# Kernel tuning notes

Measured on AMD Instinct MI355X. Metric: run time of the kernel, lower is better.

## Reference

```python
import jax, jax.numpy as jnp
import numpy as np
from jax import lax

B, T, N, H, NC = 2, 8, 512, 64, 10
NEG = -1e9
LN_EPS = 1e-5


def _gatv2(x, mask, Wl, Wr, att, b):
    # GATv2Conv (PyG semantics, eval mode): e_ij = att . leaky_relu(Wr x_i + Wl x_j),
    # softmax over source nodes j with self-loops, out_i = sum_j alpha_ij * (Wl x_j).
    # x: (B, N, Fin); mask: (N, N) bool adjacency incl. self-loops; att: (heads, C).
    heads, C = att.shape
    Bn, Nn, _ = x.shape
    xl = (x @ Wl).reshape(Bn, Nn, heads, C)  # source transform
    xr = (x @ Wr).reshape(Bn, Nn, heads, C)  # target transform
    s = jax.nn.leaky_relu(xr[:, :, None] + xl[:, None, :], 0.2)  # (B, Ni, Nj, h, C)
    e = jnp.einsum('bijhc,hc->bijh', s, att)
    e = jnp.where(mask[None, :, :, None], e, NEG)
    alpha = jax.nn.softmax(e, axis=2)  # softmax over neighbors j
    out = jnp.einsum('bijh,bjhc->bihc', alpha, xl)
    return out.reshape(Bn, Nn, heads * C) + b


def _gru_layer(x, Wih, Whh, bih, bhh):
    # torch nn.GRU single layer, batch_first; x: (B, T, Hin)
    h0 = jnp.zeros((x.shape[0], Whh.shape[0]), x.dtype)
    def step(h, xt):
        gi = xt @ Wih + bih
        gh = h @ Whh + bhh
        ir, iz, inn = jnp.split(gi, 3, axis=-1)
        hr, hz, hn = jnp.split(gh, 3, axis=-1)
        r = jax.nn.sigmoid(ir + hr)
        z = jax.nn.sigmoid(iz + hz)
        n = jnp.tanh(inn + r * hn)
        hnew = (1.0 - z) * n + z * h
        return hnew, hnew
    _, ys = lax.scan(step, h0, jnp.swapaxes(x, 0, 1))
    return jnp.swapaxes(ys, 0, 1)


def setup_inputs() -> dict:
    key = jax.random.key(0)
    ks = jax.random.split(key, 20)
    def rn(i, shape, s=0.1):
        return jax.random.normal(ks[i], shape, jnp.float32) * s
    x_seq = jax.random.normal(ks[0], (B, T, N, 1), jnp.float32)
    a = jax.random.uniform(ks[1], (N, N))
    up = jnp.triu((a > 0.95).astype(jnp.float32), 1)
    static_adj = up + up.T  # sparse symmetric 0/1 static graph
    dyn_W = jax.random.normal(ks[2], (N, N), jnp.float32)
    reg_lambda = jnp.array([0.05], jnp.float32)
    return {
        'x_seq': x_seq, 'static_adj': static_adj, 'dyn_W': dyn_W, 'reg_lambda': reg_lambda,
        'g1_Wl': rn(3, (1, H)), 'g1_Wr': rn(4, (1, H)), 'g1_att': rn(5, (4, H // 4)), 'g1_b': jnp.zeros(H),
        'g2_Wl': rn(6, (H, H)), 'g2_Wr': rn(7, (H, H)), 'g2_att': rn(8, (1, H)), 'g2_b': jnp.zeros(H),
        'gru_Wih0': rn(9, (H, 3 * H)), 'gru_Whh0': rn(10, (H, 3 * H)), 'gru_bih0': jnp.zeros(3 * H), 'gru_bhh0': jnp.zeros(3 * H),
        'gru_Wih1': rn(11, (H, 3 * H)), 'gru_Whh1': rn(12, (H, 3 * H)), 'gru_bih1': jnp.zeros(3 * H), 'gru_bhh1': jnp.zeros(3 * H),
        'attn_W': rn(13, (H, 1)), 'attn_b': jnp.zeros(1),
        'cls_W1': rn(14, (H, H)), 'cls_b1': jnp.zeros(H), 'ln_g': jnp.ones(H), 'ln_b': jnp.zeros(H),
        'cls_W2': rn(15, (H, NC)), 'cls_b2': jnp.zeros(NC),
    }


def reference(x_seq, static_adj, dyn_W, reg_lambda,
              g1_Wl, g1_Wr, g1_att, g1_b, g2_Wl, g2_Wr, g2_att, g2_b,
              gru_Wih0, gru_Whh0, gru_bih0, gru_bhh0,
              gru_Wih1, gru_Whh1, gru_bih1, gru_bhh1,
              attn_W, attn_b, cls_W1, cls_b1, ln_g, ln_b, cls_W2, cls_b2):
    Bn, Tn, Nn, _ = x_seq.shape
    lam = jnp.maximum(reg_lambda[0], 0.01)
    t = jnp.arange(Tn, dtype=x_seq.dtype)
    gts = jnp.exp(-lam * t)  # gating values per timestep
    dyn = jax.nn.relu(dyn_W + dyn_W.T)
    fused = gts[:, None, None] * static_adj + (1.0 - gts)[:, None, None] * dyn  # (T, N, N)
    masks = (fused > 0) | jnp.eye(Nn, dtype=bool)[None]  # edge set + self-loops

    def step(carry, inp):
        xt, mask = inp  # xt: (B, N, 1)
        h = jax.nn.elu(_gatv2(xt, mask, g1_Wl, g1_Wr, g1_att, g1_b))
        h = jax.nn.elu(_gatv2(h, mask, g2_Wl, g2_Wr, g2_att, g2_b))
        return carry, h.mean(axis=1)  # (B, H) graph readout

    _, reps = lax.scan(step, 0.0, (jnp.swapaxes(x_seq, 0, 1), masks))
    h_seq = jnp.swapaxes(reps, 0, 1)  # (B, T, H)

    gru_out = _gru_layer(h_seq, gru_Wih0, gru_Whh0, gru_bih0, gru_bhh0)
    gru_out = _gru_layer(gru_out, gru_Wih1, gru_Whh1, gru_bih1, gru_bhh1)

    att_scores = jax.nn.softmax((gru_out @ attn_W + attn_b)[..., 0], axis=1)  # (B, T)
    final = jnp.einsum('bt,bth->bh', att_scores, gru_out)

    z = final @ cls_W1 + cls_b1
    mu = jnp.mean(z, axis=-1, keepdims=True)
    var = jnp.var(z, axis=-1, keepdims=True)
    z = (z - mu) / jnp.sqrt(var + LN_EPS) * ln_g + ln_b
    z = jax.nn.gelu(z, approximate=False)
    logits = z @ cls_W2 + cls_b2
    return logits, gts, att_scores
```

## Files before the change

kernel.cpp:

```cpp
#include <hip/hip_runtime.h>
#include <math.h>

#define BB 2
#define TT 8
#define NN 512
#define HH 64
#define NC 10

typedef unsigned char uchar;

__device__ __forceinline__ float elu1(float v){ return v > 0.f ? v : expm1f(v); }
__device__ __forceinline__ float sigm(float v){ return 1.f/(1.f+expf(-v)); }

__global__ __launch_bounds__(256) void k_mask(
    const float* __restrict__ dW, const float* __restrict__ sadj,
    uchar* __restrict__ M0, uchar* __restrict__ M1,
    float* __restrict__ Z2, float* __restrict__ hseq,
    const float* __restrict__ att1, const float* __restrict__ Wr1,
    const float* __restrict__ Wl1, float* __restrict__ AB,
    const float* __restrict__ Whh0, const float* __restrict__ Wih1,
    const float* __restrict__ Whh1, float4* __restrict__ WT4)
{
    __shared__ float tr[64][65];
    int bx = blockIdx.x, by = blockIdx.y;
    int tid = threadIdx.x;
    if (blockIdx.z == 1){
        int idx = (by*8 + bx)*256 + tid;
        if (idx < 3*4096){
            int m = idx >> 12, r = idx & 4095;
            int gg = r >> 6, k = r & 63;
            const float* W = (m == 0) ? Whh0 : (m == 1) ? Wih1 : Whh1;
            float4 o;
            o.x = W[k*192 + gg];
            o.y = W[k*192 + 64 + gg];
            o.z = W[k*192 + 128 + gg];
            o.w = 0.f;
            WT4[(size_t)m*4096 + r] = o;
        }
        return;
    }
    int i0 = by*64, j0 = bx*64;
    #pragma unroll
    for (int q = 0; q < 4; ++q){
        int r = (tid >> 4) + 16*q, c4 = tid & 15;
        float4 v = *(const float4*)&dW[(size_t)(j0+r)*NN + i0 + 4*c4];
        tr[r][4*c4+0] = v.x; tr[r][4*c4+1] = v.y;
        tr[r][4*c4+2] = v.z; tr[r][4*c4+3] = v.w;
    }
    __syncthreads();
    #pragma unroll
    for (int q = 0; q < 4; ++q){
        int row = (tid >> 4) + 16*q, c4 = tid & 15;
        int i = i0 + row, j = j0 + 4*c4;
        float4 d  = *(const float4*)&dW[(size_t)i*NN + j];
        float4 sa = *(const float4*)&sadj[(size_t)i*NN + j];
        uchar4 m0, m1;
        float dd0 = d.x + tr[4*c4+0][row];
        float dd1 = d.y + tr[4*c4+1][row];
        float dd2 = d.z + tr[4*c4+2][row];
        float dd3 = d.w + tr[4*c4+3][row];
        m0.x = (sa.x > 0.f) || (i == j+0);
        m0.y = (sa.y > 0.f) || (i == j+1);
        m0.z = (sa.z > 0.f) || (i == j+2);
        m0.w = (sa.w > 0.f) || (i == j+3);
        m1.x = m0.x || (dd0 > 0.f);
        m1.y = m0.y || (dd1 > 0.f);
        m1.z = m0.z || (dd2 > 0.f);
        m1.w = m0.w || (dd3 > 0.f);
        *(uchar4*)&M0[(size_t)i*NN + j] = m0;
        *(uchar4*)&M1[(size_t)i*NN + j] = m1;
    }
    int flat = (by*8 + bx)*256 + tid;
    if (flat < BB*TT*NN) Z2[flat] = 0.f;
    else if (flat < BB*TT*NN + BB*TT*HH) hseq[flat - BB*TT*NN] = 0.f;
    if (bx == 0 && by == 0 && tid < 8){
        int h = tid & 3;
        const float* W = (tid < 4) ? Wr1 : Wl1;
        float s = 0.f;
        for (int c = 0; c < 16; ++c) s += att1[h*16+c]*W[h*16+c];
        AB[tid] = s;
    }
}

__global__ __launch_bounds__(256) void k_gat1f(
    const float* __restrict__ x_seq, const uchar* __restrict__ M0,
    const uchar* __restrict__ M1,
    const float* __restrict__ Wl, const float* __restrict__ Wr,
    const float* __restrict__ att, const float* __restrict__ bias,
    const float* __restrict__ AB,
    const float* __restrict__ Wl2, const float* __restrict__ Wr2,
    const float* __restrict__ att2,
    float* __restrict__ xl2, float* __restrict__ xr2,
    float* __restrict__ ui, float* __restrict__ vj)
{
    __shared__ float x_s[NN];
    __shared__ float S_s[4][4];
    __shared__ float h_s[4][HH];
    __shared__ float Wl2_s[64*64];
    __shared__ float Wr2_s[64*64];
    int bt = blockIdx.y; int t = bt % TT;
    int i0 = blockIdx.x * 4;
    int tid = threadIdx.x;
    int il = tid >> 6, jl = tid & 63;
    int i = i0 + il;
    const uchar* M = t ? M1 : M0;
    ((float2*)x_s)[tid] = ((const float2*)(x_seq + bt*NN))[tid];
    #pragma unroll
    for (int q = 0; q < 4; ++q){
        int idx = q*256 + tid;
        ((float4*)Wl2_s)[idx] = ((const float4*)Wl2)[idx];
        ((float4*)Wr2_s)[idx] = ((const float4*)Wr2)[idx];
    }
    __syncthreads();
    float xi = x_s[i];
    const uchar* Mrow = M + (size_t)i*NN;
    float xj[8], msk[8];
    #pragma unroll
    for (int jj = 0; jj < 8; ++jj){
        int j = jj*64 + jl;
        xj[jj] = x_s[j];
        msk[jj] = Mrow[j] ? 1.f : 0.f;
    }
    float sw[4] = {0,0,0,0}, swx[4] = {0,0,0,0};
    for (int h = 0; h < 4; ++h){
        float acc[8] = {0,0,0,0,0,0,0,0};
        #pragma unroll
        for (int c = 0; c < 16; ++c){
            int hc = h*16 + c;
            float wl = Wl[hc];
            float q  = 0.4f * att[hc];
            float pr = xi * Wr[hc];
            #pragma unroll
            for (int jj = 0; jj < 8; ++jj){
                float s = fmaf(xj[jj], wl, pr);
                acc[jj] = fmaf(q, fabsf(s), acc[jj]);
            }
        }
        float lin = 0.6f * xi * AB[h];
        float al6 = 0.6f * AB[4+h];
        #pragma unroll
        for (int jj = 0; jj < 8; ++jj){
            float e = acc[jj] + fmaf(al6, xj[jj], lin);
            float w = msk[jj] * __expf(e);
            sw[h] += w;
            swx[h] = fmaf(w, xj[jj], swx[h]);
        }
    }
    #pragma unroll
    for (int off = 32; off; off >>= 1){
        #pragma unroll
        for (int h = 0; h < 4; ++h){
            sw[h]  += __shfl_down(sw[h],  off);
            swx[h] += __shfl_down(swx[h], off);
        }
    }
    if (jl == 0){
        #pragma unroll
        for (int h = 0; h < 4; ++h) S_s[il][h] = swx[h] / sw[h];
    }
    __syncthreads();
    {
        int hc = tid & 63, row = tid >> 6;
        float v = S_s[row][hc >> 4] * Wl[hc] + bias[hc];
        h_s[row][hc] = elu1(v);
    }
    __syncthreads();
    {
        int c = tid & 63, row = tid >> 6;
        float al = 0.f, ar = 0.f;
        #pragma unroll 8
        for (int k = 0; k < 64; ++k){
            float hv = h_s[row][k];
            al = fmaf(hv, Wl2_s[k*64 + c], al);
            ar = fmaf(hv, Wr2_s[k*64 + c], ar);
        }
        size_t ridx = (size_t)(bt*NN + i0 + row);
        xl2[ridx*HH + c] = al;
        xr2[ridx*HH + c] = ar;
        float a2 = att2[c];
        float pu = a2 * ar, pv = a2 * al;
        #pragma unroll
        for (int off = 32; off; off >>= 1){
            pu += __shfl_down(pu, off);
            pv += __shfl_down(pv, off);
        }
        if (c == 0){ ui[ridx] = pu; vj[ridx] = pv; }
    }
}

__global__ __launch_bounds__(256) void k_e2(
    const float* __restrict__ xl2, const float* __restrict__ xr2,
    const uchar* __restrict__ M0, const uchar* __restrict__ M1,
    const float* __restrict__ att,
    const float* __restrict__ ui, const float* __restrict__ vj,
    float* __restrict__ WgT, float* __restrict__ Z2)
{
    __shared__ float xrT[64][68];
    __shared__ float xlT[64][68];
    int bt = blockIdx.z, t = bt % TT;
    int i0 = blockIdx.y*64, j0 = blockIdx.x*64;
    int base = bt*NN;
    int tid = threadIdx.x;
    const uchar* M = t ? M1 : M0;
    {
        int r = tid >> 2;
        #pragma unroll
        for (int q = 0; q < 4; ++q){
            int c4 = (tid & 3) + 4*q;
            float4 a = *(const float4*)&xr2[(size_t)(base+i0+r)*HH + 4*c4];
            float4 b = *(const float4*)&xl2[(size_t)(base+j0+r)*HH + 4*c4];
            xrT[4*c4+0][r] = a.x; xrT[4*c4+1][r] = a.y;
            xrT[4*c4+2][r] = a.z; xrT[4*c4+3][r] = a.w;
            xlT[4*c4+0][r] = b.x; xlT[4*c4+1][r] = b.y;
            xlT[4*c4+2][r] = b.z; xlT[4*c4+3][r] = b.w;
        }
    }
    int ti = tid >> 4, tj = tid & 15;
    int iL = ti*4, jL = tj*4;
    float4 u4 = *(const float4*)&ui[base+i0+iL];
    float4 v4 = *(const float4*)&vj[base+j0+jL];
    float uu[4] = {u4.x, u4.y, u4.z, u4.w};
    float vv[4] = {v4.x, v4.y, v4.z, v4.w};
    float acc[4][4];
    #pragma unroll
    for (int ii = 0; ii < 4; ++ii)
        #pragma unroll
        for (int jj = 0; jj < 4; ++jj)
            acc[ii][jj] = 0.6f*(uu[ii] + vv[jj]);
    __syncthreads();
    #pragma unroll 8
    for (int c = 0; c < 64; ++c){
        float qa = 0.4f * att[c];
        float4 a4 = *(const float4*)&xrT[c][iL];
        float4 b4 = *(const float4*)&xlT[c][jL];
        float a[4] = {a4.x, a4.y, a4.z, a4.w};
        float b[4] = {b4.x, b4.y, b4.z, b4.w};
        #pragma unroll
        for (int ii = 0; ii < 4; ++ii)
            #pragma unroll
            for (int jj = 0; jj < 4; ++jj)
                acc[ii][jj] = fmaf(qa, fabsf(a[ii] + b[jj]), acc[ii][jj]);
    }
    float w[4][4];
    #pragma unroll
    for (int ii = 0; ii < 4; ++ii){
        int i = i0 + iL + ii;
        uchar4 mr = *(const uchar4*)&M[(size_t)i*NN + j0 + jL];
        w[ii][0] = mr.x ? __expf(acc[ii][0]) : 0.f;
        w[ii][1] = mr.y ? __expf(acc[ii][1]) : 0.f;
        w[ii][2] = mr.z ? __expf(acc[ii][2]) : 0.f;
        w[ii][3] = mr.w ? __expf(acc[ii][3]) : 0.f;
    }
    #pragma unroll
    for (int jj = 0; jj < 4; ++jj){
        int j = j0 + jL + jj;
        float4 wv = { w[0][jj], w[1][jj], w[2][jj], w[3][jj] };
        *(float4*)&WgT[(size_t)(base+j)*NN + i0 + iL] = wv;
    }
    #pragma unroll
    for (int ii = 0; ii < 4; ++ii){
        float zi = w[ii][0] + w[ii][1] + w[ii][2] + w[ii][3];
        zi += __shfl_down(zi, 8);
        zi += __shfl_down(zi, 4);
        zi += __shfl_down(zi, 2);
        zi += __shfl_down(zi, 1);
        if (tj == 0) atomicAdd(&Z2[base + i0 + iL + ii], zi);
    }
}

__global__ __launch_bounds__(256) void k_a2(
    const float* __restrict__ WgT, const float* __restrict__ xl2,
    const float* __restrict__ Z2, const float* __restrict__ bias,
    float* __restrict__ hseq)
{
    __shared__ float a_s[64][20];
    __shared__ float x_s[64][68];
    __shared__ float msum[64];
    int bt = blockIdx.y;
    int i0 = blockIdx.x * 16;
    int base = bt * NN;
    int tid = threadIdx.x;
    int tg = tid >> 4, tc = tid & 15;
    if (tid < 64) msum[tid] = 0.f;
    float4 acc = {0,0,0,0};
    for (int jc = 0; jc < 8; ++jc){
        int j0 = jc*64;
        {
            int row = tid >> 2, c4 = tid & 3;
            ((float4*)&a_s[row][0])[c4] = ((const float4*)&WgT[(size_t)(base+j0+row)*NN + i0])[c4];
        }
        #pragma unroll
        for (int q = 0; q < 4; ++q){
            int idx = q*256 + tid; int row = idx >> 4, c4 = idx & 15;
            ((float4*)&x_s[row][0])[c4] = ((const float4*)&xl2[(size_t)(base+j0+row)*HH])[c4];
        }
        __syncthreads();
        #pragma unroll 8
        for (int j = 0; j < 64; ++j){
            float a = a_s[j][tg];
            float4 xv = ((float4*)&x_s[j][0])[tc];
            acc.x = fmaf(a, xv.x, acc.x);
            acc.y = fmaf(a, xv.y, acc.y);
            acc.z = fmaf(a, xv.z, acc.z);
            acc.w = fmaf(a, xv.w, acc.w);
        }
        __syncthreads();
    }
    float rz = 1.f / Z2[base + i0 + tg];
    float4 b4 = ((const float4*)bias)[tc];
    float4 h;
    h.x = elu1(acc.x*rz + b4.x);
    h.y = elu1(acc.y*rz + b4.y);
    h.z = elu1(acc.z*rz + b4.z);
    h.w = elu1(acc.w*rz + b4.w);
    atomicAdd(&msum[tc*4+0], h.x);
    atomicAdd(&msum[tc*4+1], h.y);
    atomicAdd(&msum[tc*4+2], h.z);
    atomicAdd(&msum[tc*4+3], h.w);
    __syncthreads();
    if (tid < 64) atomicAdd(&hseq[bt*HH + tid], msum[tid]*(1.f/(float)NN));
}

__global__ __launch_bounds__(256) void k_pre(
    const float* __restrict__ hseq, const float* __restrict__ Wih0,
    const float* __restrict__ bih0, float* __restrict__ gi0)
{
    int idx = blockIdx.x*256 + threadIdx.x;
    int bt = idx / 192, g = idx % 192;
    const float* x = hseq + bt*HH;
    float acc = bih0[g];
    #pragma unroll 8
    for (int k = 0; k < HH; ++k)
        acc = fmaf(x[k], Wih0[k*192 + g], acc);
    gi0[idx] = acc;
}

#define P4 65
__global__ __launch_bounds__(512) void k_gru2(
    const float* __restrict__ gi0, const float4* __restrict__ WT4,
    const float* __restrict__ bhh0,
    const float* __restrict__ bih1, const float* __restrict__ bhh1,
    const float* __restrict__ lamp, const float* __restrict__ attn_W,
    const float* __restrict__ attn_b, const float* __restrict__ W1,
    const float* __restrict__ b1, const float* __restrict__ ln_g,
    const float* __restrict__ ln_b, const float* __restrict__ W2,
    const float* __restrict__ b2, float* __restrict__ out)
{
    __shared__ float4 WA[64*P4];
    __shared__ float4 WB[64*P4];
    __shared__ float gi_s[BB*TT*192];
    __shared__ float y_s[BB*TT*HH];
    __shared__ float sc_s[BB][TT], at_s[BB][TT];
    __shared__ float fin_s[BB][HH], z_s[BB][HH], g_s[BB][HH];
    __shared__ float mu_s[BB], iv_s[BB];
    int tid = threadIdx.x;
    int wave = tid >> 6, lane = tid & 63;
    for (int v = tid; v < 4096; v += 512){
        WA[(v >> 6)*P4 + (v & 63)] = WT4[v];
        WB[(v >> 6)*P4 + (v & 63)] = WT4[4096 + v];
    }
    for (int v = tid; v < BB*TT*192; v += 512) gi_s[v] = gi0[v];
    __syncthreads();
    float y[TT];
    float g1r[TT], g1z[TT], g1n[TT];
    if (wave < 2){
        int b = wave;
        float bhr = bhh0[lane], bhz = bhh0[64+lane], bhn = bhh0[128+lane];
        float h = 0.f;
        for (int t = 0; t < TT; ++t){
            float ghr = bhr, ghz = bhz, ghn = bhn;
            #pragma unroll 16
            for (int k = 0; k < 64; ++k){
                float4 w4 = WA[lane*P4 + k];
                float hk = __shfl(h, k);
                ghr = fmaf(w4.x, hk, ghr);
                ghz = fmaf(w4.y, hk, ghz);
                ghn = fmaf(w4.z, hk, ghn);
            }
            const float* gi = &gi_s[(b*TT + t)*192];
            float r = sigm(gi[lane] + ghr);
            float z = sigm(gi[64+lane] + ghz);
            float n = tanhf(gi[128+lane] + r*ghn);
            h = (1.f - z)*n + z*h;
            y[t] = h;
        }
        float bi1r = bih1[lane], bi1z = bih1[64+lane], bi1n = bih1[128+lane];
        #pragma unroll
        for (int t = 0; t < TT; ++t){ g1r[t] = bi1r; g1z[t] = bi1z; g1n[t] = bi1n; }
        #pragma unroll 8
        for (int k = 0; k < 64; ++k){
            float4 w4 = WB[lane*P4 + k];
            #pragma unroll
            for (int t = 0; t < TT; ++t){
                float yk = __shfl(y[t], k);
                g1r[t] = fmaf(w4.x, yk, g1r[t]);
                g1z[t] = fmaf(w4.y, yk, g1z[t]);
                g1n[t] = fmaf(w4.z, yk, g1n[t]);
            }
        }
    }
    __syncthreads();
    if (wave >= 2){
        for (int v = tid - 128; v < 4096; v += 384)
            WA[(v >> 6)*P4 + (v & 63)] = WT4[2*4096 + v];
    }
    __syncthreads();
    if (wave < 2){
        int b = wave;
        float bhr = bhh1[lane], bhz = bhh1[64+lane], bhn = bhh1[128+lane];
        float h = 0.f;
        for (int t = 0; t < TT; ++t){
            float ghr = bhr, ghz = bhz, ghn = bhn;
            #pragma unroll 16
            for (int k = 0; k < 64; ++k){
                float4 w4 = WA[lane*P4 + k];
                float hk = __shfl(h, k);
                ghr = fmaf(w4.x, hk, ghr);
                ghz = fmaf(w4.y, hk, ghz);
                ghn = fmaf(w4.z, hk, ghn);
            }
            float r = sigm(g1r[t] + ghr);
            float z = sigm(g1z[t] + ghz);
            float n = tanhf(g1n[t] + r*ghn);
            h = (1.f - z)*n + z*h;
            y_s[(b*TT + t)*HH + lane] = h;
        }
    }
    __syncthreads();
    float lam = fmaxf(lamp[0], 0.01f);
    if (tid < TT) out[BB*NC + tid] = expf(-lam*(float)tid);
    if (tid < BB*TT){
        int bb = tid >> 3, t = tid & 7;
        float s = attn_b[0];
        const float* r = &y_s[(bb*TT+t)*HH];
        for (int h = 0; h < HH; ++h) s += r[h]*attn_W[h];
        sc_s[bb][t] = s;
    }
    __syncthreads();
    if (tid < BB){
        float mx = -INFINITY;
        for (int t = 0; t < TT; ++t) mx = fmaxf(mx, sc_s[tid][t]);
        float se = 0.f;
        for (int t = 0; t < TT; ++t){ float w = expf(sc_s[tid][t]-mx); at_s[tid][t] = w; se += w; }
        for (int t = 0; t < TT; ++t){
            at_s[tid][t] /= se;
            out[BB*NC + TT + tid*TT + t] = at_s[tid][t];
        }
    }
    __syncthreads();
    if (tid < BB*HH){
        int bb = tid >> 6, h = tid & 63;
        float a = 0.f;
        for (int t = 0; t < TT; ++t) a += at_s[bb][t]*y_s[(bb*TT+t)*HH + h];
        fin_s[bb][h] = a;
    }
    __syncthreads();
    if (tid < BB*HH){
        int bb = tid >> 6, h = tid & 63;
        float a = b1[h];
        for (int k = 0; k < HH; ++k) a += fin_s[bb][k]*W1[k*HH+h];
        z_s[bb][h] = a;
    }
    __syncthreads();
    if (tid < BB){
        float mu = 0.f;
        for (int h = 0; h < HH; ++h) mu += z_s[tid][h];
        mu *= (1.f/HH);
        float v = 0.f;
        for (int h = 0; h < HH; ++h){ float d = z_s[tid][h]-mu; v += d*d; }
        v *= (1.f/HH);
        mu_s[tid] = mu; iv_s[tid] = 1.f/sqrtf(v + 1e-5f);
    }
    __syncthreads();
    if (tid < BB*HH){
        int bb = tid >> 6, h = tid & 63;
        float zn = (z_s[bb][h]-mu_s[bb])*iv_s[bb]*ln_g[h] + ln_b[h];
        g_s[bb][h] = 0.5f*zn*(1.f + erff(zn*0.70710678118654752f));
    }
    __syncthreads();
    if (tid < BB*NC){
        int bb = tid / NC, c = tid % NC;
        float a = b2[c];
        for (int k = 0; k < HH; ++k) a += g_s[bb][k]*W2[k*NC+c];
        out[bb*NC + c] = a;
    }
}

extern "C" void kernel_launch(void* const* d_in, const int* in_sizes, int n_in,
                              void* d_out, int out_size, void* d_ws, size_t ws_size,
                              hipStream_t stream)
{
    const float* x_seq = (const float*)d_in[0];
    const float* sadj  = (const float*)d_in[1];
    const float* dynW  = (const float*)d_in[2];
    const float* lamp  = (const float*)d_in[3];
    const float* g1_Wl = (const float*)d_in[4];
    const float* g1_Wr = (const float*)d_in[5];
    const float* g1_att= (const float*)d_in[6];
    const float* g1_b  = (const float*)d_in[7];
    const float* g2_Wl = (const float*)d_in[8];
    const float* g2_Wr = (const float*)d_in[9];
    const float* g2_att= (const float*)d_in[10];
    const float* g2_b  = (const float*)d_in[11];
    const float* Wih0  = (const float*)d_in[12];
    const float* Whh0  = (const float*)d_in[13];
    const float* bih0  = (const float*)d_in[14];
    const float* bhh0  = (const float*)d_in[15];
    const float* Wih1  = (const float*)d_in[16];
    const float* Whh1  = (const float*)d_in[17];
    const float* bih1  = (const float*)d_in[18];
    const float* bhh1  = (const float*)d_in[19];
    const float* attnW = (const float*)d_in[20];
    const float* attnb = (const float*)d_in[21];
    const float* W1    = (const float*)d_in[22];
    const float* b1    = (const float*)d_in[23];
    const float* lng   = (const float*)d_in[24];
    const float* lnb   = (const float*)d_in[25];
    const float* W2    = (const float*)d_in[26];
    const float* b2    = (const float*)d_in[27];
    float* out = (float*)d_out;

    const int RWS = BB*TT*NN*HH;
    uchar* M0 = (uchar*)d_ws;
    uchar* M1 = M0 + (size_t)NN*NN;
    float* fb = (float*)(M1 + (size_t)NN*NN);
    float* Z2   = fb;
    float* AB   = Z2   + BB*TT*NN;
    float* ui   = AB   + 16;
    float* vj   = ui   + BB*TT*NN;
    float* xl2  = vj   + BB*TT*NN;
    float* xr2  = xl2  + RWS;
    float* WgT  = xr2  + RWS;
    float* hseq = WgT  + (size_t)BB*TT*NN*NN;
    float* gi0  = hseq + BB*TT*HH;
    float4* WT4 = (float4*)(gi0 + BB*TT*192);

    k_mask <<<dim3(8,8,2), 256, 0, stream>>>(dynW, sadj, M0, M1, Z2, hseq, g1_att, g1_Wr, g1_Wl, AB,
                                             Whh0, Wih1, Whh1, WT4);
    k_gat1f<<<dim3(NN/4, BB*TT), 256, 0, stream>>>(x_seq, M0, M1, g1_Wl, g1_Wr, g1_att, g1_b, AB,
                                                   g2_Wl, g2_Wr, g2_att, xl2, xr2, ui, vj);
    k_e2   <<<dim3(NN/64, NN/64, BB*TT), 256, 0, stream>>>(xl2, xr2, M0, M1, g2_att, ui, vj, WgT, Z2);
    k_a2   <<<dim3(NN/16, BB*TT), 256, 0, stream>>>(WgT, xl2, Z2, g2_b, hseq);
    k_pre  <<<12, 256, 0, stream>>>(hseq, Wih0, bih0, gi0);
    k_gru2 <<<1, 512, 0, stream>>>(gi0, WT4, bhh0, bih1, bhh1,
                                   lamp, attnW, attnb, W1, b1, lng, lnb, W2, b2, out);
}
```

Before: 223.0 us.

## Fuse GRU tail into aggregation kernel via last-block-done atomic counter

Folds k_pre and k_gru2 into the k_a2 aggregation kernel. An atomic completion counter lets the last finishing block run the input projection, both GRU layers, the attention and the classifier head. This removes two kernel launches and the gi0 round-trip through global memory. In exchange the GRU weights are read from global/L2 instead of being staged in LDS, and the serial tail runs on a single 256-thread block.

```diff
diff --git a/kernel.cpp b/kernel.cpp
--- a/kernel.cpp
+++ b/kernel.cpp
@@ -15,7 +15,7 @@
 __global__ __launch_bounds__(256) void k_mask(
     const float* __restrict__ dW, const float* __restrict__ sadj,
     uchar* __restrict__ M0, uchar* __restrict__ M1,
-    float* __restrict__ Z2, float* __restrict__ hseq,
+    float* __restrict__ Z2, float* __restrict__ hseq, unsigned* __restrict__ done,
     const float* __restrict__ att1, const float* __restrict__ Wr1,
     const float* __restrict__ Wl1, float* __restrict__ AB,
     const float* __restrict__ Whh0, const float* __restrict__ Wih1,
@@ -35,7 +35,7 @@
             o.y = W[k*192 + 64 + gg];
             o.z = W[k*192 + 128 + gg];
             o.w = 0.f;
-            WT4[(size_t)m*4096 + r] = o;
+            WT4[idx] = o;
         }
         return;
     }
@@ -73,6 +73,7 @@
     int flat = (by*8 + bx)*256 + tid;
     if (flat < BB*TT*NN) Z2[flat] = 0.f;
     else if (flat < BB*TT*NN + BB*TT*HH) hseq[flat - BB*TT*NN] = 0.f;
+    else if (flat == BB*TT*NN + BB*TT*HH) done[0] = 0u;
     if (bx == 0 && by == 0 && tid < 8){
         int h = tid & 3;
         const float* W = (tid < 4) ? Wr1 : Wl1;
@@ -268,14 +269,24 @@
     }
 }
 
-__global__ __launch_bounds__(256) void k_a2(
+__global__ __launch_bounds__(256, 4) void k_a2t(
     const float* __restrict__ WgT, const float* __restrict__ xl2,
     const float* __restrict__ Z2, const float* __restrict__ bias,
-    float* __restrict__ hseq)
+    float* __restrict__ hseq, unsigned* __restrict__ done,
+    const float* __restrict__ Wih0, const float* __restrict__ bih0,
+    const float4* __restrict__ WT4, const float* __restrict__ bhh0,
+    const float* __restrict__ bih1, const float* __restrict__ bhh1,
+    const float* __restrict__ lamp, const float* __restrict__ attn_W,
+    const float* __restrict__ attn_b, const float* __restrict__ W1,
+    const float* __restrict__ b1, const float* __restrict__ ln_g,
+    const float* __restrict__ ln_b, const float* __restrict__ W2,
+    const float* __restrict__ b2, float* __restrict__ out)
 {
-    __shared__ float a_s[64][20];
-    __shared__ float x_s[64][68];
-    __shared__ float msum[64];
+    __shared__ __align__(16) float S[5696];
+    __shared__ unsigned isLast;
+    float* a_s  = S;
+    float* x_s  = S + 1280;
+    float* msum = S + 5632;
     int bt = blockIdx.y;
     int i0 = blockIdx.x * 16;
     int base = bt * NN;
@@ -287,18 +298,18 @@
         int j0 = jc*64;
         {
             int row = tid >> 2, c4 = tid & 3;
-            ((float4*)&a_s[row][0])[c4] = ((const float4*)&WgT[(size_t)(base+j0+row)*NN + i0])[c4];
+            *(float4*)&a_s[row*20 + 4*c4] = *(const float4*)&WgT[(size_t)(base+j0+row)*NN + i0 + 4*c4];
         }
         #pragma unroll
         for (int q = 0; q < 4; ++q){
             int idx = q*256 + tid; int row = idx >> 4, c4 = idx & 15;
-            ((float4*)&x_s[row][0])[c4] = ((const float4*)&xl2[(size_t)(base+j0+row)*HH])[c4];
+            *(float4*)&x_s[row*68 + 4*c4] = *(const float4*)&xl2[(size_t)(base+j0+row)*HH + 4*c4];
         }
         __syncthreads();
         #pragma unroll 8
         for (int j = 0; j < 64; ++j){
-            float a = a_s[j][tg];
-            float4 xv = ((float4*)&x_s[j][0])[tc];
+            float a = a_s[j*20 + tg];
+            float4 xv = *(const float4*)&x_s[j*68 + 4*tc];
             acc.x = fmaf(a, xv.x, acc.x);
             acc.y = fmaf(a, xv.y, acc.y);
             acc.z = fmaf(a, xv.z, acc.z);
@@ -313,175 +324,164 @@
     h.y = elu1(acc.y*rz + b4.y);
     h.z = elu1(acc.z*rz + b4.z);
     h.w = elu1(acc.w*rz + b4.w);
-    atomicAdd(&msum[tc*4+0], h.x);
-    atomicAdd(&msum[tc*4+1], h.y);
-    atomicAdd(&msum[tc*4+2], h.z);
-    atomicAdd(&msum[tc*4+3], h.w);
+    atomicAdd(&msum[4*tc+0], h.x);
+    atomicAdd(&msum[4*tc+1], h.y);
+    atomicAdd(&msum[4*tc+2], h.z);
+    atomicAdd(&msum[4*tc+3], h.w);
     __syncthreads();
     if (tid < 64) atomicAdd(&hseq[bt*HH + tid], msum[tid]*(1.f/(float)NN));
-}
-
-__global__ __launch_bounds__(256) void k_pre(
-    const float* __restrict__ hseq, const float* __restrict__ Wih0,
-    const float* __restrict__ bih0, float* __restrict__ gi0)
-{
-    int idx = blockIdx.x*256 + threadIdx.x;
-    int bt = idx / 192, g = idx % 192;
-    const float* x = hseq + bt*HH;
-    float acc = bih0[g];
-    #pragma unroll 8
-    for (int k = 0; k < HH; ++k)
-        acc = fmaf(x[k], Wih0[k*192 + g], acc);
-    gi0[idx] = acc;
-}
-
-#define P4 65
-__global__ __launch_bounds__(512) void k_gru2(
-    const float* __restrict__ gi0, const float4* __restrict__ WT4,
-    const float* __restrict__ bhh0,
-    const float* __restrict__ bih1, const float* __restrict__ bhh1,
-    const float* __restrict__ lamp, const float* __restrict__ attn_W,
-    const float* __restrict__ attn_b, const float* __restrict__ W1,
-    const float* __restrict__ b1, const float* __restrict__ ln_g,
-    const float* __restrict__ ln_b, const float* __restrict__ W2,
-    const float* __restrict__ b2, float* __restrict__ out)
-{
-    __shared__ float4 WA[64*P4];
-    __shared__ float4 WB[64*P4];
-    __shared__ float gi_s[BB*TT*192];
-    __shared__ float y_s[BB*TT*HH];
-    __shared__ float sc_s[BB][TT], at_s[BB][TT];
-    __shared__ float fin_s[BB][HH], z_s[BB][HH], g_s[BB][HH];
-    __shared__ float mu_s[BB], iv_s[BB];
-    int tid = threadIdx.x;
+    if (tid == 0){
+        __threadfence();
+        unsigned old = __hip_atomic_fetch_add(done, 1u, __ATOMIC_ACQ_REL, __HIP_MEMORY_SCOPE_AGENT);
+        isLast = (old == 32u*16u - 1u) ? 1u : 0u;
+        if (isLast) __threadfence();
+    }
+    __syncthreads();
+    if (!isLast) return;
+    float* hs   = S;
+    float* gi_s = S + 1024;
+    float* y_s  = S + 4096;
+    float* sc_s = S + 5120;
+    float* at_s = S + 5136;
+    float* fin_s= S + 5152;
+    float* z_s  = S + 5280;
+    float* g_s  = S + 5408;
+    float* mu_s = S + 5536;
+    float* iv_s = S + 5538;
+    __syncthreads();
+    for (int o = tid; o < BB*TT*HH; o += 256)
+        hs[o] = __hip_atomic_load(&hseq[o], __ATOMIC_RELAXED, __HIP_MEMORY_SCOPE_AGENT);
+    __syncthreads();
+    for (int o = tid; o < BB*TT*192; o += 256){
+        int b = o / 192, g = o % 192;
+        float a = bih0[g];
+        #pragma unroll 8
+        for (int k = 0; k < HH; ++k)
+            a = fmaf(hs[b*HH + k], Wih0[k*192 + g], a);
+        gi_s[o] = a;
+    }
+    __syncthreads();
     int wave = tid >> 6, lane = tid & 63;
-    for (int v = tid; v < 4096; v += 512){
-        WA[(v >> 6)*P4 + (v & 63)] = WT4[v];
-        WB[(v >> 6)*P4 + (v & 63)] = WT4[4096 + v];
-    }
-    for (int v = tid; v < BB*TT*192; v += 512) gi_s[v] = gi0[v];
-    __syncthreads();
-    float y[TT];
-    float g1r[TT], g1z[TT], g1n[TT];
     if (wave < 2){
         int b = wave;
-        float bhr = bhh0[lane], bhz = bhh0[64+lane], bhn = bhh0[128+lane];
-        float h = 0.f;
-        for (int t = 0; t < TT; ++t){
-            float ghr = bhr, ghz = bhz, ghn = bhn;
-            #pragma unroll 16
+        float y[TT], g1r[TT], g1z[TT], g1n[TT];
+        {
+            float bhr = bhh0[lane], bhz = bhh0[64+lane], bhn = bhh0[128+lane];
+            float hh = 0.f;
+            for (int tt = 0; tt < TT; ++tt){
+                float ghr = bhr, ghz = bhz, ghn = bhn;
+                #pragma unroll 8
+                for (int k = 0; k < 64; ++k){
+                    float4 w4 = WT4[lane*64 + k];
+                    float hk = __shfl(hh, k);
+                    ghr = fmaf(w4.x, hk, ghr);
+                    ghz = fmaf(w4.y, hk, ghz);
+                    ghn = fmaf(w4.z, hk, ghn);
+                }
+                const float* gi = &gi_s[(b*TT + tt)*192];
+                float r = sigm(gi[lane] + ghr);
+                float z = sigm(gi[64+lane] + ghz);
+                float n = tanhf(gi[128+lane] + r*ghn);
+                hh = (1.f - z)*n + z*hh;
+                y[tt] = hh;
+            }
+        }
+        {
+            float bi1r = bih1[lane], bi1z = bih1[64+lane], bi1n = bih1[128+lane];
+            #pragma unroll
+            for (int tt = 0; tt < TT; ++tt){ g1r[tt] = bi1r; g1z[tt] = bi1z; g1n[tt] = bi1n; }
+            #pragma unroll 4
             for (int k = 0; k < 64; ++k){
-                float4 w4 = WA[lane*P4 + k];
-                float hk = __shfl(h, k);
-                ghr = fmaf(w4.x, hk, ghr);
-                ghz = fmaf(w4.y, hk, ghz);
-                ghn = fmaf(w4.z, hk, ghn);
+                float4 w4 = WT4[4096 + lane*64 + k];
+                #pragma unroll
+                for (int tt = 0; tt < TT; ++tt){
+                    float yk = __shfl(y[tt], k);
+                    g1r[tt] = fmaf(w4.x, yk, g1r[tt]);
+                    g1z[tt] = fmaf(w4.y, yk, g1z[tt]);
+                    g1n[tt] = fmaf(w4.z, yk, g1n[tt]);
+                }
             }
-            const float* gi = &gi_s[(b*TT + t)*192];
-            float r = sigm(gi[lane] + ghr);
-            float z = sigm(gi[64+lane] + ghz);
-            float n = tanhf(gi[128+lane] + r*ghn);
-            h = (1.f - z)*n + z*h;
-            y[t] = h;
-        }
-        float bi1r = bih1[lane], bi1z = bih1[64+lane], bi1n = bih1[128+lane];
-        #pragma unroll
-        for (int t = 0; t < TT; ++t){ g1r[t] = bi1r; g1z[t] = bi1z; g1n[t] = bi1n; }
-        #pragma unroll 8
-        for (int k = 0; k < 64; ++k){
-            float4 w4 = WB[lane*P4 + k];
-            #pragma unroll
-            for (int t = 0; t < TT; ++t){
-                float yk = __shfl(y[t], k);
-                g1r[t] = fmaf(w4.x, yk, g1r[t]);
-                g1z[t] = fmaf(w4.y, yk, g1z[t]);
-                g1n[t] = fmaf(w4.z, yk, g1n[t]);
+        }
+        {
+            float bhr = bhh1[lane], bhz = bhh1[64+lane], bhn = bhh1[128+lane];
+            float hh = 0.f;
+            for (int tt = 0; tt < TT; ++tt){
+                float ghr = bhr, ghz = bhz, ghn = bhn;
+                #pragma unroll 8
+                for (int k = 0; k < 64; ++k){
+                    float4 w4 = WT4[2*4096 + lane*64 + k];
+                    float hk = __shfl(hh, k);
+                    ghr = fmaf(w4.x, hk, ghr);
+                    ghz = fmaf(w4.y, hk, ghz);
+                    ghn = fmaf(w4.z, hk, ghn);
+                }
+                float r = sigm(g1r[tt] + ghr);
+                float z = sigm(g1z[tt] + ghz);
+                float n = tanhf(g1n[tt] + r*ghn);
+                hh = (1.f - z)*n + z*hh;
+                y_s[(b*TT + tt)*HH + lane] = hh;
             }
-        }
-    }
-    __syncthreads();
-    if (wave >= 2){
-        for (int v = tid - 128; v < 4096; v += 384)
-            WA[(v >> 6)*P4 + (v & 63)] = WT4[2*4096 + v];
-    }
-    __syncthreads();
-    if (wave < 2){
-        int b = wave;
-        float bhr = bhh1[lane], bhz = bhh1[64+lane], bhn = bhh1[128+lane];
-        float h = 0.f;
-        for (int t = 0; t < TT; ++t){
-            float ghr = bhr, ghz = bhz, ghn = bhn;
-            #pragma unroll 16
-            for (int k = 0; k < 64; ++k){
-                float4 w4 = WA[lane*P4 + k];
-                float hk = __shfl(h, k);
-                ghr = fmaf(w4.x, hk, ghr);
-                ghz = fmaf(w4.y, hk, ghz);
-                ghn = fmaf(w4.z, hk, ghn);
-            }
-            float r = sigm(g1r[t] + ghr);
-            float z = sigm(g1z[t] + ghz);
-            float n = tanhf(g1n[t] + r*ghn);
-            h = (1.f - z)*n + z*h;
-            y_s[(b*TT + t)*HH + lane] = h;
         }
     }
     __syncthreads();
     float lam = fmaxf(lamp[0], 0.01f);
     if (tid < TT) out[BB*NC + tid] = expf(-lam*(float)tid);
     if (tid < BB*TT){
-        int bb = tid >> 3, t = tid & 7;
+        int bb = tid >> 3, tt = tid & 7;
         float s = attn_b[0];
-        const float* r = &y_s[(bb*TT+t)*HH];
-        for (int h = 0; h < HH; ++h) s += r[h]*attn_W[h];
-        sc_s[bb][t] = s;
+        const float* r = &y_s[(bb*TT+tt)*HH];
+        for (int hh = 0; hh < HH; ++hh) s += r[hh]*attn_W[hh];
+        sc_s[bb*TT + tt] = s;
     }
     __syncthreads();
     if (tid < BB){
         float mx = -INFINITY;
-        for (int t = 0; t < TT; ++t) mx = fmaxf(mx, sc_s[tid][t]);
+        for (int tt = 0; tt < TT; ++tt) mx = fmaxf(mx, sc_s[tid*TT + tt]);
         float se = 0.f;
-        for (int t = 0; t < TT; ++t){ float w = expf(sc_s[tid][t]-mx); at_s[tid][t] = w; se += w; }
-        for (int t = 0; t < TT; ++t){
-            at_s[tid][t] /= se;
-            out[BB*NC + TT + tid*TT + t] = at_s[tid][t];
+        for (int tt = 0; tt < TT; ++tt){
+            float w = expf(sc_s[tid*TT + tt] - mx);
+            at_s[tid*TT + tt] = w; se += w;
+        }
+        for (int tt = 0; tt < TT; ++tt){
+            at_s[tid*TT + tt] /= se;
+            out[BB*NC + TT + tid*TT + tt] = at_s[tid*TT + tt];
         }
     }
     __syncthreads();
     if (tid < BB*HH){
-        int bb = tid >> 6, h = tid & 63;
+        int bb = tid >> 6, hh = tid & 63;
         float a = 0.f;
-        for (int t = 0; t < TT; ++t) a += at_s[bb][t]*y_s[(bb*TT+t)*HH + h];
-        fin_s[bb][h] = a;
+        for (int tt = 0; tt < TT; ++tt) a += at_s[bb*TT + tt]*y_s[(bb*TT+tt)*HH + hh];
+        fin_s[bb*HH + hh] = a;
     }
     __syncthreads();
     if (tid < BB*HH){
-        int bb = tid >> 6, h = tid & 63;
-        float a = b1[h];
-        for (int k = 0; k < HH; ++k) a += fin_s[bb][k]*W1[k*HH+h];
-        z_s[bb][h] = a;
+        int bb = tid >> 6, hh = tid & 63;
+        float a = b1[hh];
+        for (int k = 0; k < HH; ++k) a += fin_s[bb*HH + k]*W1[k*HH+hh];
+        z_s[bb*HH + hh] = a;
     }
     __syncthreads();
     if (tid < BB){
         float mu = 0.f;
-        for (int h = 0; h < HH; ++h) mu += z_s[tid][h];
+        for (int hh = 0; hh < HH; ++hh) mu += z_s[tid*HH + hh];
         mu *= (1.f/HH);
         float v = 0.f;
-        for (int h = 0; h < HH; ++h){ float d = z_s[tid][h]-mu; v += d*d; }
+        for (int hh = 0; hh < HH; ++hh){ float d = z_s[tid*HH + hh]-mu; v += d*d; }
         v *= (1.f/HH);
         mu_s[tid] = mu; iv_s[tid] = 1.f/sqrtf(v + 1e-5f);
     }
     __syncthreads();
     if (tid < BB*HH){
-        int bb = tid >> 6, h = tid & 63;
-        float zn = (z_s[bb][h]-mu_s[bb])*iv_s[bb]*ln_g[h] + ln_b[h];
-        g_s[bb][h] = 0.5f*zn*(1.f + erff(zn*0.70710678118654752f));
+        int bb = tid >> 6, hh = tid & 63;
+        float zn = (z_s[bb*HH + hh]-mu_s[bb])*iv_s[bb]*ln_g[hh] + ln_b[hh];
+        g_s[bb*HH + hh] = 0.5f*zn*(1.f + erff(zn*0.70710678118654752f));
     }
     __syncthreads();
     if (tid < BB*NC){
         int bb = tid / NC, c = tid % NC;
         float a = b2[c];
-        for (int k = 0; k < HH; ++k) a += g_s[bb][k]*W2[k*NC+c];
+        for (int k = 0; k < HH; ++k) a += g_s[bb*HH + k]*W2[k*NC+c];
         out[bb*NC + c] = a;
     }
 }
@@ -532,16 +532,17 @@
     float* xr2  = xl2  + RWS;
     float* WgT  = xr2  + RWS;
     float* hseq = WgT  + (size_t)BB*TT*NN*NN;
-    float* gi0  = hseq + BB*TT*HH;
-    float4* WT4 = (float4*)(gi0 + BB*TT*192);
-
-    k_mask <<<dim3(8,8,2), 256, 0, stream>>>(dynW, sadj, M0, M1, Z2, hseq, g1_att, g1_Wr, g1_Wl, AB,
-                                             Whh0, Wih1, Whh1, WT4);
+    float* WT4  = hseq + BB*TT*HH;
+    unsigned* done = (unsigned*)(WT4 + 3*4096*4);
+
+    k_mask <<<dim3(8,8,2), 256, 0, stream>>>(dynW, sadj, M0, M1, Z2, hseq, done,
+                                             g1_att, g1_Wr, g1_Wl, AB,
+                                             Whh0, Wih1, Whh1, (float4*)WT4);
     k_gat1f<<<dim3(NN/4, BB*TT), 256, 0, stream>>>(x_seq, M0, M1, g1_Wl, g1_Wr, g1_att, g1_b, AB,
                                                    g2_Wl, g2_Wr, g2_att, xl2, xr2, ui, vj);
     k_e2   <<<dim3(NN/64, NN/64, BB*TT), 256, 0, stream>>>(xl2, xr2, M0, M1, g2_att, ui, vj, WgT, Z2);
-    k_a2   <<<dim3(NN/16, BB*TT), 256, 0, stream>>>(WgT, xl2, Z2, g2_b, hseq);
-    k_pre  <<<12, 256, 0, stream>>>(hseq, Wih0, bih0, gi0);
-    k_gru2 <<<1, 512, 0, stream>>>(gi0, WT4, bhh0, bih1, bhh1,
-                                   lamp, attnW, attnb, W1, b1, lng, lnb, W2, b2, out);
+    k_a2t  <<<dim3(NN/16, BB*TT), 256, 0, stream>>>(WgT, xl2, Z2, g2_b, hseq, done,
+                                                    Wih0, bih0, (const float4*)WT4, bhh0,
+                                                    bih1, bhh1, lamp, attnW, attnb,
+                                                    W1, b1, lng, lnb, W2, b2, out);
 }
```

New measurement: 303.7 us. +36.2%, slower.
